# Kernel tuning notes

Hardware: AMD Instinct MI355X
Metric: run time of the kernel (lower is better)

Reference implementation:

```python
import jax, jax.numpy as jnp
import numpy as np

N_NODES = 100000
N_EDGES = 1200000
N_GRAPHS = 1024
IN_DIM, HIDDEN, OUT_DIM = 4, 64, 2
BN_EPS = 1e-5


def setup_inputs() -> dict:
    key = jax.random.key(0)
    ks = jax.random.split(key, 12)
    x = jax.random.normal(ks[0], (N_NODES, IN_DIM), dtype=jnp.float32)
    edge_index = jax.random.randint(ks[1], (2, N_EDGES), 0, N_NODES, dtype=jnp.int64)
    batch = jnp.sort(jax.random.randint(ks[2], (N_NODES,), 0, N_GRAPHS, dtype=jnp.int64))
    s = 1.0 / np.sqrt(HIDDEN)
    return {
        "x": x,
        "edge_index": edge_index,
        "batch": batch,
        "W_enc": jax.random.normal(ks[3], (IN_DIM, HIDDEN), dtype=jnp.float32) * 0.5,
        "b_enc": jnp.zeros((HIDDEN,), dtype=jnp.float32),
        "bn_gamma": jnp.ones((HIDDEN,), dtype=jnp.float32),
        "bn_beta": jnp.zeros((HIDDEN,), dtype=jnp.float32),
        "bn_mean": jax.random.normal(ks[4], (HIDDEN,), dtype=jnp.float32) * 0.1,
        "bn_var": jax.random.uniform(ks[5], (HIDDEN,), dtype=jnp.float32, minval=0.5, maxval=1.5),
        "W_gcn": jax.random.normal(ks[6], (HIDDEN, HIDDEN), dtype=jnp.float32) * s,
        "b_gcn": jnp.zeros((HIDDEN,), dtype=jnp.float32),
        "W_cls1": jax.random.normal(ks[7], (HIDDEN, HIDDEN), dtype=jnp.float32) * s,
        "b_cls1": jnp.zeros((HIDDEN,), dtype=jnp.float32),
        "W_cls2": jax.random.normal(ks[8], (HIDDEN, OUT_DIM), dtype=jnp.float32) * s,
        "b_cls2": jnp.zeros((OUT_DIM,), dtype=jnp.float32),
    }


def reference(x, edge_index, batch, W_enc, b_enc, bn_gamma, bn_beta, bn_mean, bn_var,
              W_gcn, b_gcn, W_cls1, b_cls1, W_cls2, b_cls2):
    n = x.shape[0]
    # Encoder: Linear -> ReLU -> Dropout(eval=identity) -> BatchNorm1d (running stats)
    h = jnp.maximum(x @ W_enc + b_enc, 0.0)
    h = (h - bn_mean) * jax.lax.rsqrt(bn_var + BN_EPS) * bn_gamma + bn_beta
    # GCNConv (PyG): add self-loops, symmetric deg^{-1/2} normalization
    loop = jnp.arange(n, dtype=edge_index.dtype)
    src = jnp.concatenate([edge_index[0], loop])  # [E+N]
    dst = jnp.concatenate([edge_index[1], loop])
    deg = jnp.zeros((n,), dtype=h.dtype).at[dst].add(1.0)
    dis = jnp.where(deg > 0, jax.lax.rsqrt(jnp.maximum(deg, 1.0)), 0.0)
    norm = dis[src] * dis[dst]  # [E+N]
    hw = h @ W_gcn  # [N, H]
    msg = hw[src] * norm[:, None]  # gather + scale, [E+N, H]
    agg = jax.ops.segment_sum(msg, dst, num_segments=n) + b_gcn
    agg = jnp.maximum(agg, 0.0)  # .relu()
    # global_mean_pool over graphs
    sums = jax.ops.segment_sum(agg, batch, num_segments=N_GRAPHS)  # [G, H]
    cnts = jax.ops.segment_sum(jnp.ones((n,), dtype=agg.dtype), batch, num_segments=N_GRAPHS)
    gm = sums / jnp.maximum(cnts, 1.0)[:, None]
    # Classifier: Linear -> ReLU -> Dropout(eval) -> Linear
    out = jnp.maximum(gm @ W_cls1 + b_cls1, 0.0) @ W_cls2 + b_cls2
    return out
```

## Files before the change

kernel.cpp:

```cpp
#include <hip/hip_runtime.h>

#define N_NODES  100000
#define N_EDGES  1200000
#define N_GRAPHS 1024

#define BSH    8
#define BNODES 256
#define NBUCK  391
#define BCAP   4096
#define BINB   512
#define CHUNK  ((N_EDGES + BINB - 1) / BINB)
#define ENCB   1563

__device__ __forceinline__ unsigned short f2bf(float f) {
  unsigned u = __float_as_uint(f);
  return (unsigned short)((u + 0x7fffu + ((u >> 16) & 1u)) >> 16);
}
__device__ __forceinline__ float bf2f(unsigned short b) {
  return __uint_as_float(((unsigned)b) << 16);
}

__global__ __launch_bounds__(256) void k_zero(float* __restrict__ gsum,
                                              int* __restrict__ cur) {
  int i = blockIdx.x * 256 + threadIdx.x;
  gsum[i] = 0.f;
  if (i < NBUCK) cur[i] = 0;
}

__global__ __launch_bounds__(256) void k_binenc(
    const int* __restrict__ ei, int* __restrict__ cur, int* __restrict__ binned,
    const float* __restrict__ x,
    const float* __restrict__ Wenc, const float* __restrict__ benc,
    const float* __restrict__ gamma, const float* __restrict__ beta,
    const float* __restrict__ mean,  const float* __restrict__ var,
    const float* __restrict__ Wgcn,
    unsigned short* __restrict__ hw) {
  int t = threadIdx.x;
  int lane = t & 63, w = t >> 6;
  if (blockIdx.x < BINB) {
    __shared__ int h[NBUCK];
    int blk = blockIdx.x;
    for (int i = t; i < NBUCK; i += 256) h[i] = 0;
    __syncthreads();
    int start = blk * CHUNK, end = min(start + CHUNK, N_EDGES);
    for (int e = start + 4 * t; e < end; e += 4 * 256) {
      int4 d4 = *(const int4*)&ei[N_EDGES + e];
      atomicAdd(&h[d4.x >> BSH], 1);
      atomicAdd(&h[d4.y >> BSH], 1);
      atomicAdd(&h[d4.z >> BSH], 1);
      atomicAdd(&h[d4.w >> BSH], 1);
    }
    __syncthreads();
    for (int b = t; b < NBUCK; b += 256) {
      int v = h[b];
      if (v) h[b] = atomicAdd(&cur[b], v);
    }
    __syncthreads();
    for (int e = start + 4 * t; e < end; e += 4 * 256) {
      int4 s4 = *(const int4*)&ei[e];
      int4 d4 = *(const int4*)&ei[N_EDGES + e];
      int b, p;
      b = d4.x >> BSH; p = atomicAdd(&h[b], 1);
      if (p < BCAP) binned[b * BCAP + p] = s4.x | ((d4.x & (BNODES - 1)) << 17);
      b = d4.y >> BSH; p = atomicAdd(&h[b], 1);
      if (p < BCAP) binned[b * BCAP + p] = s4.y | ((d4.y & (BNODES - 1)) << 17);
      b = d4.z >> BSH; p = atomicAdd(&h[b], 1);
      if (p < BCAP) binned[b * BCAP + p] = s4.z | ((d4.z & (BNODES - 1)) << 17);
      b = d4.w >> BSH; p = atomicAdd(&h[b], 1);
      if (p < BCAP) binned[b * BCAP + p] = s4.w | ((d4.w & (BNODES - 1)) << 17);
    }
    return;
  }
  int wv = (blockIdx.x - BINB) * 4 + w;
  if (wv >= 6250) return;
  float be = benc[lane];
  float sc = gamma[lane] * rsqrtf(var[lane] + 1e-5f);
  float mu = mean[lane], bt = beta[lane];
  float w0 = Wenc[lane], w1 = Wenc[64 + lane], w2 = Wenc[128 + lane], w3 = Wenc[192 + lane];
  float wreg[64];
  #pragma unroll
  for (int k = 0; k < 64; ++k) wreg[k] = Wgcn[k * 64 + lane];
  int n0 = wv * 16;
  for (int i = 0; i < 16; ++i) {
    int n = n0 + i;
    float4 xv = ((const float4*)x)[n];
    float h = fmaf(xv.w, w3, fmaf(xv.z, w2, fmaf(xv.y, w1, fmaf(xv.x, w0, be))));
    h = fmaxf(h, 0.f);
    float hbn = (h - mu) * sc + bt;
    int hb = __float_as_int(hbn);
    float a0 = 0.f, a1 = 0.f, a2 = 0.f, a3 = 0.f;
    #pragma unroll
    for (int k = 0; k < 64; k += 4) {
      a0 = fmaf(__int_as_float(__builtin_amdgcn_readlane(hb, k)),     wreg[k],     a0);
      a1 = fmaf(__int_as_float(__builtin_amdgcn_readlane(hb, k + 1)), wreg[k + 1], a1);
      a2 = fmaf(__int_as_float(__builtin_amdgcn_readlane(hb, k + 2)), wreg[k + 2], a2);
      a3 = fmaf(__int_as_float(__builtin_amdgcn_readlane(hb, k + 3)), wreg[k + 3], a3);
    }
    hw[(size_t)n * 64 + lane] = f2bf((a0 + a1) + (a2 + a3));
  }
}

__global__ __launch_bounds__(256) void k_csr(const int* __restrict__ cur,
                                             const int* __restrict__ binned,
                                             int* __restrict__ csr,
                                             unsigned* __restrict__ rowinfo,
                                             float* __restrict__ dis) {
  __shared__ int hist[BNODES];
  __shared__ int wsum[4];
  int t = threadIdx.x, blk = blockIdx.x;
  int lane = t & 63, w = t >> 6;
  int nE = min(cur[blk], BCAP);
  int b0 = blk * BCAP;
  hist[t] = 0;
  __syncthreads();
  for (int i = t; i < nE; i += 256)
    atomicAdd(&hist[(unsigned)binned[b0 + i] >> 17], 1);
  __syncthreads();
  int v = hist[t];
  int incl = v;
  #pragma unroll
  for (int off = 1; off < 64; off <<= 1) {
    int y = __shfl_up(incl, off);
    if (lane >= off) incl += y;
  }
  if (lane == 63) wsum[w] = incl;
  __syncthreads();
  if (t == 0) {
    int s = 0;
    #pragma unroll
    for (int i = 0; i < 4; ++i) { int x2 = wsum[i]; wsum[i] = s; s += x2; }
  }
  __syncthreads();
  int excl = wsum[w] + incl - v;
  hist[t] = excl;
  int node = (blk << BSH) + t;
  if (node < N_NODES) {
    rowinfo[node] = (unsigned)(b0 + excl) | ((unsigned)v << 21);
    dis[node] = rsqrtf((float)(v + 1));
  }
  __syncthreads();
  for (int i = t; i < nE; i += 256) {
    int vv = binned[b0 + i];
    int p = atomicAdd(&hist[(unsigned)vv >> 17], 1);
    csr[b0 + p] = vv & 0x1FFFF;
  }
}

__global__ __launch_bounds__(64) void k_gather(
    const unsigned* __restrict__ rowinfo, const int* __restrict__ csr,
    const float* __restrict__ dis, const unsigned short* __restrict__ hw,
    const int* __restrict__ batch, const float* __restrict__ bgcn,
    float* __restrict__ gsum) {
  int lane = threadIdx.x;
  int nb = blockIdx.x * 4;
  float bias = bgcn[lane];
  float vout[4];
  int gid[4];
  #pragma unroll
  for (int k = 0; k < 4; ++k) {
    int n = nb + k;
    unsigned u = rowinfo[n];
    int st = (int)(u & 0x1FFFFF);
    int v  = (int)(u >> 21);
    int en = st + v;
    float dn = rsqrtf((float)(v + 1));
    float a0 = 0.f, a1 = 0.f, a2 = 0.f, a3 = 0.f;
    for (int c = st; c < en; c += 64) {
      int m = min(64, en - c);
      int idx = c + lane;
      int chunk = 0; float dv = 0.f;
      if (idx < en) { chunk = csr[idx]; dv = dis[chunk]; }
      int dvb = __float_as_int(dv);
      int j = 0;
      for (; j + 4 <= m; j += 4) {
        int s0 = __builtin_amdgcn_readlane(chunk, j);
        int s1 = __builtin_amdgcn_readlane(chunk, j + 1);
        int s2 = __builtin_amdgcn_readlane(chunk, j + 2);
        int s3 = __builtin_amdgcn_readlane(chunk, j + 3);
        float d0 = __int_as_float(__builtin_amdgcn_readlane(dvb, j));
        float d1 = __int_as_float(__builtin_amdgcn_readlane(dvb, j + 1));
        float d2 = __int_as_float(__builtin_amdgcn_readlane(dvb, j + 2));
        float d3 = __int_as_float(__builtin_amdgcn_readlane(dvb, j + 3));
        a0 = fmaf(d0, bf2f(hw[(size_t)s0 * 64 + lane]), a0);
        a1 = fmaf(d1, bf2f(hw[(size_t)s1 * 64 + lane]), a1);
        a2 = fmaf(d2, bf2f(hw[(size_t)s2 * 64 + lane]), a2);
        a3 = fmaf(d3, bf2f(hw[(size_t)s3 * 64 + lane]), a3);
      }
      for (; j < m; ++j) {
        int s = __builtin_amdgcn_readlane(chunk, j);
        float d = __int_as_float(__builtin_amdgcn_readlane(dvb, j));
        a0 = fmaf(d, bf2f(hw[(size_t)s * 64 + lane]), a0);
      }
    }
    float self = bf2f(hw[(size_t)n * 64 + lane]);
    float sum = (a0 + a1) + (a2 + a3);
    vout[k] = fmaxf(dn * fmaf(dn, self, sum) + bias, 0.f);
    gid[k] = batch[n];
  }
  float vs = vout[0];
  int cg = gid[0];
  #pragma unroll
  for (int k = 1; k < 4; ++k) {
    if (gid[k] == cg) vs += vout[k];
    else {
      atomicAdd(&gsum[cg * 64 + lane], vs);
      vs = vout[k]; cg = gid[k];
    }
  }
  atomicAdd(&gsum[cg * 64 + lane], vs);
}

__global__ void k_cls(const float* __restrict__ gsum, const int* __restrict__ batch,
                      const float* __restrict__ W1, const float* __restrict__ b1,
                      const float* __restrict__ W2, const float* __restrict__ b2,
                      float* __restrict__ out) {
  __shared__ float gm[64];
  __shared__ int cntS;
  int j = threadIdx.x;
  int g = blockIdx.x;
  if (j == 0) {
    int lo = 0, hi = N_NODES;
    while (lo < hi) { int mid = (lo + hi) >> 1; if (batch[mid] < g) lo = mid + 1; else hi = mid; }
    int lo2 = lo, hi2 = N_NODES;
    while (lo2 < hi2) { int mid = (lo2 + hi2) >> 1; if (batch[mid] < g + 1) lo2 = mid + 1; else hi2 = mid; }
    cntS = lo2 - lo;
  }
  __syncthreads();
  float denom = fmaxf((float)cntS, 1.0f);
  gm[j] = gsum[g * 64 + j] / denom;
  __syncthreads();
  float hid = b1[j];
  #pragma unroll
  for (int k = 0; k < 64; ++k) hid += gm[k] * W1[k * 64 + j];
  hid = fmaxf(hid, 0.f);
  float o0 = hid * W2[j * 2 + 0];
  float o1 = hid * W2[j * 2 + 1];
  #pragma unroll
  for (int off = 32; off > 0; off >>= 1) {
    o0 += __shfl_down(o0, off);
    o1 += __shfl_down(o1, off);
  }
  if (j == 0) {
    out[g * 2 + 0] = o0 + b2[0];
    out[g * 2 + 1] = o1 + b2[1];
  }
}

extern "C" void kernel_launch(void* const* d_in, const int* in_sizes, int n_in,
                              void* d_out, int out_size, void* d_ws, size_t ws_size,
                              hipStream_t stream) {
  const float* x     = (const float*)d_in[0];
  const int*   ei    = (const int*)d_in[1];
  const int*   batch = (const int*)d_in[2];
  const float* Wenc  = (const float*)d_in[3];
  const float* benc  = (const float*)d_in[4];
  const float* gamma = (const float*)d_in[5];
  const float* beta  = (const float*)d_in[6];
  const float* mean  = (const float*)d_in[7];
  const float* var   = (const float*)d_in[8];
  const float* Wgcn  = (const float*)d_in[9];
  const float* bgcn  = (const float*)d_in[10];
  const float* W1    = (const float*)d_in[11];
  const float* b1    = (const float*)d_in[12];
  const float* W2    = (const float*)d_in[13];
  const float* b2    = (const float*)d_in[14];
  float* out = (float*)d_out;

  char* ws = (char*)d_ws;
  float*          gsum    = (float*)ws;          ws += (size_t)N_GRAPHS * 64 * 4;
  int*            cur     = (int*)ws;            ws += (size_t)1024 * 4;
  int*            binned  = (int*)ws;            ws += (size_t)NBUCK * BCAP * 4;
  int*            csr     = (int*)ws;            ws += (size_t)NBUCK * BCAP * 4;
  unsigned*       rowinfo = (unsigned*)ws;       ws += (size_t)(N_NODES + 32) * 4;
  float*          dis     = (float*)ws;          ws += (size_t)N_NODES * 4;
  unsigned short* hw      = (unsigned short*)ws; ws += (size_t)N_NODES * 64 * 2;

  k_zero<<<256, 256, 0, stream>>>(gsum, cur);
  k_binenc<<<BINB + ENCB, 256, 0, stream>>>(ei, cur, binned, x, Wenc, benc,
                                            gamma, beta, mean, var, Wgcn, hw);
  k_csr<<<NBUCK, 256, 0, stream>>>(cur, binned, csr, rowinfo, dis);
  k_gather<<<(N_NODES / 4), 64, 0, stream>>>(rowinfo, csr, dis, hw, batch, bgcn, gsum);
  k_cls<<<N_GRAPHS, 64, 0, stream>>>(gsum, batch, W1, b1, W2, b2, out);
}
```

Baseline: 191.3 us.

## Fuse CSR build and gather into one LDS-sorted aggregation kernel per bucket

```diff
diff --git a/kernel.cpp b/kernel.cpp
--- a/kernel.cpp
+++ b/kernel.cpp
@@ -11,6 +11,7 @@
 #define BINB   512
 #define CHUNK  ((N_EDGES + BINB - 1) / BINB)
 #define ENCB   1563
+#define AGGT   1024
 
 __device__ __forceinline__ unsigned short f2bf(float f) {
   unsigned u = __float_as_uint(f);
@@ -21,14 +22,17 @@
 }
 
 __global__ __launch_bounds__(256) void k_zero(float* __restrict__ gsum,
+                                              int* __restrict__ deg,
                                               int* __restrict__ cur) {
   int i = blockIdx.x * 256 + threadIdx.x;
-  gsum[i] = 0.f;
+  if (i < N_GRAPHS * 64) gsum[i] = 0.f;
+  if (i < N_NODES) deg[i] = 0;
   if (i < NBUCK) cur[i] = 0;
 }
 
 __global__ __launch_bounds__(256) void k_binenc(
     const int* __restrict__ ei, int* __restrict__ cur, int* __restrict__ binned,
+    int* __restrict__ deg,
     const float* __restrict__ x,
     const float* __restrict__ Wenc, const float* __restrict__ benc,
     const float* __restrict__ gamma, const float* __restrict__ beta,
@@ -45,10 +49,10 @@
     int start = blk * CHUNK, end = min(start + CHUNK, N_EDGES);
     for (int e = start + 4 * t; e < end; e += 4 * 256) {
       int4 d4 = *(const int4*)&ei[N_EDGES + e];
-      atomicAdd(&h[d4.x >> BSH], 1);
-      atomicAdd(&h[d4.y >> BSH], 1);
-      atomicAdd(&h[d4.z >> BSH], 1);
-      atomicAdd(&h[d4.w >> BSH], 1);
+      atomicAdd(&h[d4.x >> BSH], 1); atomicAdd(&deg[d4.x], 1);
+      atomicAdd(&h[d4.y >> BSH], 1); atomicAdd(&deg[d4.y], 1);
+      atomicAdd(&h[d4.z >> BSH], 1); atomicAdd(&deg[d4.z], 1);
+      atomicAdd(&h[d4.w >> BSH], 1); atomicAdd(&deg[d4.w], 1);
     }
     __syncthreads();
     for (int b = t; b < NBUCK; b += 256) {
@@ -100,30 +104,48 @@
   }
 }
 
-__global__ __launch_bounds__(256) void k_csr(const int* __restrict__ cur,
-                                             const int* __restrict__ binned,
-                                             int* __restrict__ csr,
-                                             unsigned* __restrict__ rowinfo,
-                                             float* __restrict__ dis) {
+__global__ __launch_bounds__(AGGT) void k_agg(
+    const int* __restrict__ cur, const int* __restrict__ binned,
+    const int* __restrict__ deg, const unsigned short* __restrict__ hw,
+    const int* __restrict__ batch, const float* __restrict__ bgcn,
+    float* __restrict__ gsum) {
+  __shared__ int raw[BCAP];
+  __shared__ int srt[BCAP];
   __shared__ int hist[BNODES];
+  __shared__ int rs[BNODES];
   __shared__ int wsum[4];
   int t = threadIdx.x, blk = blockIdx.x;
   int lane = t & 63, w = t >> 6;
   int nE = min(cur[blk], BCAP);
   int b0 = blk * BCAP;
-  hist[t] = 0;
-  __syncthreads();
-  for (int i = t; i < nE; i += 256)
-    atomicAdd(&hist[(unsigned)binned[b0 + i] >> 17], 1);
-  __syncthreads();
-  int v = hist[t];
-  int incl = v;
-  #pragma unroll
-  for (int off = 1; off < 64; off <<= 1) {
-    int y = __shfl_up(incl, off);
-    if (lane >= off) incl += y;
-  }
-  if (lane == 63) wsum[w] = incl;
+  if (t < BNODES) hist[t] = 0;
+  __syncthreads();
+  int nE4 = nE & ~3;
+  for (int i = 4 * t; i < nE4; i += 4 * AGGT) {
+    int4 v4 = *(const int4*)&binned[b0 + i];
+    *(int4*)&raw[i] = v4;
+    atomicAdd(&hist[(unsigned)v4.x >> 17], 1);
+    atomicAdd(&hist[(unsigned)v4.y >> 17], 1);
+    atomicAdd(&hist[(unsigned)v4.z >> 17], 1);
+    atomicAdd(&hist[(unsigned)v4.w >> 17], 1);
+  }
+  for (int i = nE4 + t; i < nE; i += AGGT) {
+    int v = binned[b0 + i];
+    raw[i] = v;
+    atomicAdd(&hist[(unsigned)v >> 17], 1);
+  }
+  __syncthreads();
+  int v = 0, incl = 0;
+  if (t < BNODES) {
+    v = hist[t];
+    incl = v;
+    #pragma unroll
+    for (int off = 1; off < 64; off <<= 1) {
+      int y = __shfl_up(incl, off);
+      if (lane >= off) incl += y;
+    }
+    if (lane == 63) wsum[w] = incl;
+  }
   __syncthreads();
   if (t == 0) {
     int s = 0;
@@ -131,45 +153,37 @@
     for (int i = 0; i < 4; ++i) { int x2 = wsum[i]; wsum[i] = s; s += x2; }
   }
   __syncthreads();
-  int excl = wsum[w] + incl - v;
-  hist[t] = excl;
-  int node = (blk << BSH) + t;
-  if (node < N_NODES) {
-    rowinfo[node] = (unsigned)(b0 + excl) | ((unsigned)v << 21);
-    dis[node] = rsqrtf((float)(v + 1));
-  }
-  __syncthreads();
-  for (int i = t; i < nE; i += 256) {
-    int vv = binned[b0 + i];
+  if (t < BNODES) {
+    int excl = wsum[w] + incl - v;
+    rs[t] = excl;
+    hist[t] = excl;
+  }
+  __syncthreads();
+  for (int i = t; i < nE; i += AGGT) {
+    int vv = raw[i];
     int p = atomicAdd(&hist[(unsigned)vv >> 17], 1);
-    csr[b0 + p] = vv & 0x1FFFF;
-  }
-}
-
-__global__ __launch_bounds__(64) void k_gather(
-    const unsigned* __restrict__ rowinfo, const int* __restrict__ csr,
-    const float* __restrict__ dis, const unsigned short* __restrict__ hw,
-    const int* __restrict__ batch, const float* __restrict__ bgcn,
-    float* __restrict__ gsum) {
-  int lane = threadIdx.x;
-  int nb = blockIdx.x * 4;
+    srt[p] = vv & 0x1FFFF;
+  }
+  __syncthreads();
+  int node0 = blk << BSH;
   float bias = bgcn[lane];
-  float vout[4];
-  int gid[4];
-  #pragma unroll
-  for (int k = 0; k < 4; ++k) {
-    int n = nb + k;
-    unsigned u = rowinfo[n];
-    int st = (int)(u & 0x1FFFFF);
-    int v  = (int)(u >> 21);
-    int en = st + v;
-    float dn = rsqrtf((float)(v + 1));
+  float vs = 0.f;
+  int cg = -1;
+  for (int k = 0; k < 16; ++k) {
+    int nl = w * 16 + k;
+    int n = node0 + nl;
+    if (n >= N_NODES) break;
+    int st = rs[nl], en = hist[nl];
+    float dn = rsqrtf((float)(en - st) + 1.f);
     float a0 = 0.f, a1 = 0.f, a2 = 0.f, a3 = 0.f;
     for (int c = st; c < en; c += 64) {
       int m = min(64, en - c);
       int idx = c + lane;
       int chunk = 0; float dv = 0.f;
-      if (idx < en) { chunk = csr[idx]; dv = dis[chunk]; }
+      if (idx < en) {
+        chunk = srt[idx];
+        dv = rsqrtf((float)deg[chunk] + 1.f);
+      }
       int dvb = __float_as_int(dv);
       int j = 0;
       for (; j + 4 <= m; j += 4) {
@@ -194,20 +208,15 @@
     }
     float self = bf2f(hw[(size_t)n * 64 + lane]);
     float sum = (a0 + a1) + (a2 + a3);
-    vout[k] = fmaxf(dn * fmaf(dn, self, sum) + bias, 0.f);
-    gid[k] = batch[n];
-  }
-  float vs = vout[0];
-  int cg = gid[0];
-  #pragma unroll
-  for (int k = 1; k < 4; ++k) {
-    if (gid[k] == cg) vs += vout[k];
+    float o = fmaxf(dn * fmaf(dn, self, sum) + bias, 0.f);
+    int g = batch[n];
+    if (g == cg) vs += o;
     else {
-      atomicAdd(&gsum[cg * 64 + lane], vs);
-      vs = vout[k]; cg = gid[k];
-    }
-  }
-  atomicAdd(&gsum[cg * 64 + lane], vs);
+      if (cg >= 0) atomicAdd(&gsum[cg * 64 + lane], vs);
+      vs = o; cg = g;
+    }
+  }
+  if (cg >= 0) atomicAdd(&gsum[cg * 64 + lane], vs);
 }
 
 __global__ void k_cls(const float* __restrict__ gsum, const int* __restrict__ batch,
@@ -267,18 +276,15 @@
   float* out = (float*)d_out;
 
   char* ws = (char*)d_ws;
-  float*          gsum    = (float*)ws;          ws += (size_t)N_GRAPHS * 64 * 4;
-  int*            cur     = (int*)ws;            ws += (size_t)1024 * 4;
-  int*            binned  = (int*)ws;            ws += (size_t)NBUCK * BCAP * 4;
-  int*            csr     = (int*)ws;            ws += (size_t)NBUCK * BCAP * 4;
-  unsigned*       rowinfo = (unsigned*)ws;       ws += (size_t)(N_NODES + 32) * 4;
-  float*          dis     = (float*)ws;          ws += (size_t)N_NODES * 4;
-  unsigned short* hw      = (unsigned short*)ws; ws += (size_t)N_NODES * 64 * 2;
-
-  k_zero<<<256, 256, 0, stream>>>(gsum, cur);
-  k_binenc<<<BINB + ENCB, 256, 0, stream>>>(ei, cur, binned, x, Wenc, benc,
+  float*          gsum   = (float*)ws;          ws += (size_t)N_GRAPHS * 64 * 4;
+  int*            deg    = (int*)ws;            ws += (size_t)N_NODES * 4;
+  int*            cur    = (int*)ws;            ws += (size_t)1024 * 4;
+  int*            binned = (int*)ws;            ws += (size_t)NBUCK * BCAP * 4;
+  unsigned short* hw     = (unsigned short*)ws; ws += (size_t)N_NODES * 64 * 2;
+
+  k_zero<<<391, 256, 0, stream>>>(gsum, deg, cur);
+  k_binenc<<<BINB + ENCB, 256, 0, stream>>>(ei, cur, binned, deg, x, Wenc, benc,
                                             gamma, beta, mean, var, Wgcn, hw);
-  k_csr<<<NBUCK, 256, 0, stream>>>(cur, binned, csr, rowinfo, dis);
-  k_gather<<<(N_NODES / 4), 64, 0, stream>>>(rowinfo, csr, dis, hw, batch, bgcn, gsum);
+  k_agg<<<NBUCK, AGGT, 0, stream>>>(cur, binned, deg, hw, batch, bgcn, gsum);
   k_cls<<<N_GRAPHS, 64, 0, stream>>>(gsum, batch, W1, b1, W2, b2, out);
 }
```

Measured after the change: 232.3 us. 21.4% more time.
